# Kernel optimization log

Hardware: AMD Instinct MI355X
Metric: run time of the kernel (lower is better)

The kernel has to match this reference:

```python
import jax, jax.numpy as jnp
import numpy as np

BN_EPS = 1e-5

def batchnorm(x, gamma, beta):
    # training-mode BatchNorm1d over the row (node/sample) dimension
    mu = jnp.mean(x, axis=0)
    var = jnp.var(x, axis=0)
    return (x - mu) * jax.lax.rsqrt(var + BN_EPS) * gamma + beta

def gin_mean(h, src, dst, n):
    # DGL GINConv(apply_func=None, aggregator='mean', eps=0):
    # h_new = h + mean_{u in N(v)} h_u
    ones = jnp.ones((src.shape[0],), h.dtype)
    deg = jax.ops.segment_sum(ones, dst, num_segments=n)
    agg = jax.ops.segment_sum(h[src], dst, num_segments=n)
    return h + agg / jnp.maximum(deg, 1.0)[:, None]

def setup_inputs() -> dict:
    key = jax.random.key(0)
    ks = jax.random.split(key, 12)
    N, E, B, K = 10000, 160000, 64, 10
    DIN, D, DH = 20, 512, 256
    x = jax.random.normal(ks[0], (N, DIN), dtype=jnp.float32)
    edge_src = jax.random.randint(ks[1], (E,), 0, N, dtype=jnp.int32)
    edge_dst = jax.random.randint(ks[2], (E,), 0, N, dtype=jnp.int32)
    node2graph = jnp.sort(jax.random.randint(ks[3], (N,), 0, B, dtype=jnp.int32))
    pg_emb = jax.random.normal(ks[4], (B, D), dtype=jnp.float32)
    neigh_emb = jax.random.normal(ks[5], (B, K, D), dtype=jnp.float32)
    s = lambda i, shp: jax.random.normal(ks[i], shp, dtype=jnp.float32) * 0.02
    return dict(
        x=x, pg_emb=pg_emb, neigh_emb=neigh_emb,
        W_init=s(6, (DIN, D)), b_init=jnp.zeros((D,), jnp.float32),
        g1=jnp.ones((D,), jnp.float32), be1=jnp.zeros((D,), jnp.float32),
        g2=jnp.ones((D,), jnp.float32), be2=jnp.zeros((D,), jnp.float32),
        W_fc=s(7, (3 * D, DH)), b_fc=jnp.zeros((DH,), jnp.float32),
        W_fc2=s(8, (DH, DH)), b_fc2=jnp.zeros((DH,), jnp.float32),
        W_fc3=s(9, (DH, DH)), b_fc3=jnp.zeros((DH,), jnp.float32),
        W_fc4=s(10, (DH, 1)), b_fc4=jnp.zeros((1,), jnp.float32),
        gb=jnp.ones((DH,), jnp.float32), bb=jnp.zeros((DH,), jnp.float32),
        gb2=jnp.ones((DH,), jnp.float32), bb2=jnp.zeros((DH,), jnp.float32),
        gb3=jnp.ones((DH,), jnp.float32), bb3=jnp.zeros((DH,), jnp.float32),
        edge_src=edge_src, edge_dst=edge_dst, node2graph=node2graph,
    )

def reference(x, pg_emb, neigh_emb, W_init, b_init, g1, be1, g2, be2,
              W_fc, b_fc, W_fc2, b_fc2, W_fc3, b_fc3, W_fc4, b_fc4,
              gb, bb, gb2, bb2, gb3, bb3, edge_src, edge_dst, node2graph):
    N = x.shape[0]
    B, K, D = neigh_emb.shape
    # two GIN(mean) layers with BN+ReLU on the batched graph
    h = x @ W_init + b_init                                   # [N, 512]
    h = jax.nn.relu(batchnorm(gin_mean(h, edge_src, edge_dst, N), g1, be1))
    h = jax.nn.relu(batchnorm(gin_mean(h, edge_src, edge_dst, N), g2, be2))
    # dgl.mean_nodes: per-graph mean readout
    cnt = jax.ops.segment_sum(jnp.ones((N,), h.dtype), node2graph, num_segments=B)
    qemb = jax.ops.segment_sum(h, node2graph, num_segments=B) / jnp.maximum(cnt, 1.0)[:, None]
    a = jnp.concatenate([qemb, pg_emb], axis=1)               # [B, 2D]
    a = jnp.broadcast_to(a[:, None, :], (B, K, 2 * D))        # repeat per candidate
    b = jnp.concatenate([a, neigh_emb], axis=-1).reshape(B * K, 3 * D)
    H = jax.nn.relu(batchnorm(b @ W_fc + b_fc, gb, bb))
    H2 = jax.nn.relu(batchnorm(H @ W_fc2 + b_fc2, gb2, bb2))
    H3 = jax.nn.relu(batchnorm(H2 @ W_fc3 + b_fc3, gb3, bb3))
    pred = jax.nn.sigmoid(H3 @ W_fc4 + b_fc4)                 # [B*K, 1]
    return pred.reshape(B, K)
```

## Files before the change

kernel.cpp:

```cpp
#include <hip/hip_runtime.h>
#include <hip/hip_bf16.h>
#include <math.h>

#define N_NODES 10000
#define N_EDGES 160000
#define D 512
#define DIN 20
#define B 64
#define KC 10
#define DH 256
#define NROW (B*KC)
#define BN_EPS 1e-5f

__device__ __forceinline__ void f4acc(float4& a, const float4 v){
  a.x += v.x; a.y += v.y; a.z += v.z; a.w += v.w;
}
__device__ __forceinline__ void mk_affine(const float4 s, const float4 q, const float4 g,
                                          const float4 b, float4& sc, float4& sh){
  const float invN = 1.0f/(float)N_NODES;
  float mu, var, rs;
  mu = s.x*invN; var = q.x*invN - mu*mu; rs = rsqrtf(var+BN_EPS); sc.x = rs*g.x; sh.x = b.x - mu*sc.x;
  mu = s.y*invN; var = q.y*invN - mu*mu; rs = rsqrtf(var+BN_EPS); sc.y = rs*g.y; sh.y = b.y - mu*sc.y;
  mu = s.z*invN; var = q.z*invN - mu*mu; rs = rsqrtf(var+BN_EPS); sc.z = rs*g.z; sh.z = b.z - mu*sc.z;
  mu = s.w*invN; var = q.w*invN - mu*mu; rs = rsqrtf(var+BN_EPS); sc.w = rs*g.w; sh.w = b.w - mu*sc.w;
}
__device__ __forceinline__ float4 aff_relu(const float4 v, const float4 sc, const float4 sh){
  float4 o;
  o.x = fmaxf(fmaf(v.x, sc.x, sh.x), 0.0f);
  o.y = fmaxf(fmaf(v.y, sc.y, sh.y), 0.0f);
  o.z = fmaxf(fmaf(v.z, sc.z, sh.z), 0.0f);
  o.w = fmaxf(fmaf(v.w, sc.w, sh.w), 0.0f);
  return o;
}
__device__ __forceinline__ void bf_unpack(const uint4 u, float4& lo, float4& hi){
  lo.x = __uint_as_float(u.x << 16); lo.y = __uint_as_float(u.x & 0xffff0000u);
  lo.z = __uint_as_float(u.y << 16); lo.w = __uint_as_float(u.y & 0xffff0000u);
  hi.x = __uint_as_float(u.z << 16); hi.y = __uint_as_float(u.z & 0xffff0000u);
  hi.z = __uint_as_float(u.w << 16); hi.w = __uint_as_float(u.w & 0xffff0000u);
}
__device__ __forceinline__ unsigned bf_pack2(float a, float b){
  unsigned ua = __float_as_uint(a); ua = (ua + 0x7fffu + ((ua>>16)&1u)) >> 16;
  unsigned ub = __float_as_uint(b); ub = (ub + 0x7fffu + ((ub>>16)&1u)) & 0xffff0000u;
  return (ua & 0xffffu) | ub;
}
__device__ __forceinline__ unsigned short bf_pack1(float a){
  unsigned ua = __float_as_uint(a); return (unsigned short)((ua + 0x7fffu + ((ua>>16)&1u)) >> 16);
}

#define ZCOUNT 36352
#define Z4 (ZCOUNT/4)
#define D4 (N_NODES/4)
#define SETUP_ZBLK ((Z4 + D4 + 255)/256)
__global__ void setup_kernel(const int* __restrict__ n2g, int* __restrict__ gstart,
                             float* __restrict__ zbuf, int* __restrict__ degi){
  if (blockIdx.x == SETUP_ZBLK){
    int g = threadIdx.x;
    if (g > B) return;
    int lo = 0, hi = N_NODES;
    while (lo < hi){ int mid = (lo+hi)>>1; if (n2g[mid] < g) lo = mid+1; else hi = mid; }
    gstart[g] = lo;
    return;
  }
  int i4 = blockIdx.x*256 + threadIdx.x;
  if (i4 < Z4){
    ((float4*)zbuf)[i4] = make_float4(0.f,0.f,0.f,0.f);
  } else {
    int j = i4 - Z4;
    if (j < D4) ((int4*)degi)[j] = make_int4(0,0,0,0);
  }
}

__global__ void deg_kernel(const int* __restrict__ dst, int* __restrict__ degi, int E){
  int i = blockIdx.x*blockDim.x + threadIdx.x;
  if (i < E) atomicAdd(&degi[dst[i]], 1);
}

__global__ void scan_kernel(const int* __restrict__ degi, int* __restrict__ rowstart,
                            int* __restrict__ cursor){
  __shared__ int part[256];
  int t = threadIdx.x;
  const int PER = (N_NODES + 255)/256;
  int base = t*PER;
  int s = 0;
  for (int i = 0; i < PER; ++i){
    int idx = base+i;
    if (idx < N_NODES) s += degi[idx];
  }
  part[t] = s;
  __syncthreads();
  for (int off = 1; off < 256; off <<= 1){
    int v = (t >= off) ? part[t-off] : 0;
    __syncthreads();
    part[t] += v;
    __syncthreads();
  }
  int run = (t > 0) ? part[t-1] : 0;
  for (int i = 0; i < PER; ++i){
    int idx = base+i;
    if (idx < N_NODES){
      rowstart[idx] = run; cursor[idx] = run; run += degi[idx];
    }
  }
  if (t == 255) rowstart[N_NODES] = run;
}

__global__ void fill_kernel(const int* __restrict__ src, const int* __restrict__ dst,
                            int* __restrict__ cursor, int* __restrict__ csr, int E){
  int i = blockIdx.x*blockDim.x + threadIdx.x;
  if (i < E){
    int p = atomicAdd(&cursor[dst[i]], 1);
    csr[p] = src[i];
  }
}

#define IM_ROWS 8
__global__ __launch_bounds__(256)
void init_mm_kernel(const float* __restrict__ x, const float* __restrict__ W,
                    const float* __restrict__ b, unsigned short* __restrict__ hb){
  __shared__ float Ws[DIN][D];
  __shared__ float xs[IM_ROWS][DIN];
  int t = threadIdx.x;
  int r0 = blockIdx.x*IM_ROWS;
  for (int i = t; i < DIN*D; i += 256) Ws[i >> 9][i & (D-1)] = W[i];
  for (int i = t; i < IM_ROWS*DIN; i += 256) xs[i/DIN][i%DIN] = x[(size_t)r0*DIN + i];
  __syncthreads();
  float b0 = b[t], b1 = b[t+256];
  for (int rr = 0; rr < IM_ROWS; ++rr){
    float a0 = b0, a1 = b1;
    #pragma unroll
    for (int k = 0; k < DIN; ++k){
      float xv = xs[rr][k];
      a0 += xv*Ws[k][t];
      a1 += xv*Ws[k][t+256];
    }
    hb[(size_t)(r0+rr)*D + t]       = bf_pack1(a0);
    hb[(size_t)(r0+rr)*D + t + 256] = bf_pack1(a1);
  }
}

#define GWAVES 4
#define NPW 4
#define NWAVETOT (N_NODES/NPW)
template<bool FUSED>
__global__ __launch_bounds__(256, 2)
void gin_gather_kernel(const unsigned short* __restrict__ hb,
                       const int* __restrict__ rowstart,
                       const int* __restrict__ csr,
                       const float* __restrict__ pcsum, const float* __restrict__ pcsq,
                       const float* __restrict__ pgam, const float* __restrict__ pbet,
                       unsigned short* __restrict__ h2b,
                       float* __restrict__ csum, float* __restrict__ csq){
  __shared__ float red[GWAVES][1024];
  int lane = threadIdx.x & 63;
  int wave = threadIdx.x >> 6;
  int wid  = blockIdx.x*GWAVES + wave;
  const uint4* hb4 = (const uint4*)hb;
  float4 scA, shA, scB, shB;
  if (FUSED){
    mk_affine(((const float4*)pcsum)[2*lane],   ((const float4*)pcsq)[2*lane],
              ((const float4*)pgam)[2*lane],    ((const float4*)pbet)[2*lane],   scA, shA);
    mk_affine(((const float4*)pcsum)[2*lane+1], ((const float4*)pcsq)[2*lane+1],
              ((const float4*)pgam)[2*lane+1],  ((const float4*)pbet)[2*lane+1], scB, shB);
  }
  float4 sLo = make_float4(0,0,0,0), sHi = make_float4(0,0,0,0);
  float4 qLo = make_float4(0,0,0,0), qHi = make_float4(0,0,0,0);
  for (int nn = 0; nn < NPW; ++nn){
    int node = wid + nn*NWAVETOT;
    int start = rowstart[node], end = rowstart[node+1];
    float4 aLo = make_float4(0,0,0,0), aHi = make_float4(0,0,0,0);
    float4 bLo = make_float4(0,0,0,0), bHi = make_float4(0,0,0,0);
    for (int base = start; base < end; base += 64){
      int cnt = end - base; if (cnt > 64) cnt = 64;
      int myidx = (lane < cnt) ? csr[base+lane] : 0;
      int j = 0;
      for (; j+8 <= cnt; j += 8){
        uint4 u[8];
        #pragma unroll
        for (int k = 0; k < 8; ++k){
          int idx = __shfl(myidx, j+k, 64);
          u[k] = hb4[(size_t)idx*64 + lane];
        }
        #pragma unroll
        for (int k = 0; k < 8; ++k){
          float4 lo, hi; bf_unpack(u[k], lo, hi);
          if (FUSED){ lo = aff_relu(lo, scA, shA); hi = aff_relu(hi, scB, shB); }
          if (k & 1){ f4acc(bLo, lo); f4acc(bHi, hi); }
          else      { f4acc(aLo, lo); f4acc(aHi, hi); }
        }
      }
      for (; j < cnt; ++j){
        int idx = __shfl(myidx, j, 64);
        uint4 u0 = hb4[(size_t)idx*64 + lane];
        float4 lo, hi; bf_unpack(u0, lo, hi);
        if (FUSED){ lo = aff_relu(lo, scA, shA); hi = aff_relu(hi, scB, shB); }
        f4acc(aLo, lo); f4acc(aHi, hi);
      }
    }
    float inv = 1.0f/fmaxf((float)(end-start), 1.0f);
    uint4 us = hb4[(size_t)node*64 + lane];
    float4 hLo, hHi; bf_unpack(us, hLo, hHi);
    if (FUSED){ hLo = aff_relu(hLo, scA, shA); hHi = aff_relu(hHi, scB, shB); }
    float4 oLo, oHi;
    oLo.x = hLo.x + (aLo.x+bLo.x)*inv;  oLo.y = hLo.y + (aLo.y+bLo.y)*inv;
    oLo.z = hLo.z + (aLo.z+bLo.z)*inv;  oLo.w = hLo.w + (aLo.w+bLo.w)*inv;
    oHi.x = hHi.x + (aHi.x+bHi.x)*inv;  oHi.y = hHi.y + (aHi.y+bHi.y)*inv;
    oHi.z = hHi.z + (aHi.z+bHi.z)*inv;  oHi.w = hHi.w + (aHi.w+bHi.w)*inv;
    uint4 ou;
    ou.x = bf_pack2(oLo.x, oLo.y); ou.y = bf_pack2(oLo.z, oLo.w);
    ou.z = bf_pack2(oHi.x, oHi.y); ou.w = bf_pack2(oHi.z, oHi.w);
    ((uint4*)h2b)[(size_t)node*64 + lane] = ou;
    f4acc(sLo, oLo); f4acc(sHi, oHi);
    qLo.x += oLo.x*oLo.x; qLo.y += oLo.y*oLo.y; qLo.z += oLo.z*oLo.z; qLo.w += oLo.w*oLo.w;
    qHi.x += oHi.x*oHi.x; qHi.y += oHi.y*oHi.y; qHi.z += oHi.z*oHi.z; qHi.w += oHi.w*oHi.w;
  }
  float* my = red[wave];
  int c = 8*lane;
  *((float4*)&my[c])      = sLo;  *((float4*)&my[c+4])     = sHi;
  *((float4*)&my[512+c])  = qLo;  *((float4*)&my[512+c+4]) = qHi;
  __syncthreads();
  for (int e = threadIdx.x; e < 1024; e += 256){
    float v = red[0][e] + red[1][e] + red[2][e] + red[3][e];
    if (e < 512) atomicAdd(&csum[e], v);
    else         atomicAdd(&csq[e-512], v);
  }
}

__global__ void readout_kernel(const unsigned short* __restrict__ hb,
                               const float* __restrict__ csum, const float* __restrict__ csq,
                               const float* __restrict__ gam, const float* __restrict__ bet,
                               const int* __restrict__ gstart, float* __restrict__ qemb){
  __shared__ float red[4][512];
  int g = blockIdx.x, chunk = blockIdx.y;
  int lane = threadIdx.x & 63, wave = threadIdx.x >> 6;
  const uint4* hb4 = (const uint4*)hb;
  float4 scA, shA, scB, shB;
  mk_affine(((const float4*)csum)[2*lane],   ((const float4*)csq)[2*lane],
            ((const float4*)gam)[2*lane],    ((const float4*)bet)[2*lane],   scA, shA);
  mk_affine(((const float4*)csum)[2*lane+1], ((const float4*)csq)[2*lane+1],
            ((const float4*)gam)[2*lane+1],  ((const float4*)bet)[2*lane+1], scB, shB);
  int s = gstart[g], e = gstart[g+1];
  int rows = e - s;
  int per = (rows + 7)/8;
  int r0 = s + chunk*per;
  int r1 = r0 + per; if (r1 > e) r1 = e;
  float4 aLo = make_float4(0,0,0,0), aHi = make_float4(0,0,0,0);
  for (int r = r0 + wave; r < r1; r += 4){
    uint4 u = hb4[(size_t)r*64 + lane];
    float4 lo, hi; bf_unpack(u, lo, hi);
    lo = aff_relu(lo, scA, shA); hi = aff_relu(hi, scB, shB);
    f4acc(aLo, lo); f4acc(aHi, hi);
  }
  int c = 8*lane;
  *((float4*)&red[wave][c])   = aLo;
  *((float4*)&red[wave][c+4]) = aHi;
  __syncthreads();
  for (int e2 = threadIdx.x; e2 < 512; e2 += 256){
    float v = red[0][e2] + red[1][e2] + red[2][e2] + red[3][e2];
    atomicAdd(&qemb[(size_t)g*D + e2], v);
  }
}

#define F1_ROWS 8
#define F1_KS 256
#define F1_NS 6
__global__ __launch_bounds__(256)
void fc1_partial_kernel(const float* __restrict__ qemb, const int* __restrict__ gstart,
                        const float* __restrict__ pg, const float* __restrict__ neigh,
                        const float* __restrict__ W, float* __restrict__ part){
  __shared__ float brow[F1_ROWS][F1_KS];
  int t = threadIdx.x;
  int r0 = blockIdx.x*F1_ROWS;
  int k0 = blockIdx.y*F1_KS;
  for (int rr=0; rr<F1_ROWS; ++rr){
    int r = r0+rr;
    int g = r/KC, k = r - g*KC;
    int j = k0 + t;
    float v;
    if (j < D){
      float invc = 1.0f/fmaxf((float)(gstart[g+1]-gstart[g]), 1.0f);
      v = qemb[(size_t)g*D + j]*invc;
    } else if (j < 2*D){
      v = pg[(size_t)g*D + (j-D)];
    } else {
      v = neigh[((size_t)g*KC + k)*D + (j-2*D)];
    }
    brow[rr][t] = v;
  }
  __syncthreads();
  float acc[F1_ROWS] = {0.f,0.f,0.f,0.f,0.f,0.f,0.f,0.f};
  #pragma unroll 4
  for (int kk=0; kk<F1_KS; ++kk){
    float w = W[(size_t)(k0+kk)*DH + t];
    #pragma unroll
    for (int rr=0; rr<F1_ROWS; ++rr) acc[rr] += brow[rr][kk]*w;
  }
  for (int rr=0; rr<F1_ROWS; ++rr)
    part[((size_t)blockIdx.y*NROW + r0+rr)*DH + t] = acc[rr];
}

__global__ __launch_bounds__(256)
void reduce_stats_kernel(const float* __restrict__ part, const float* __restrict__ bias,
                         float* __restrict__ out, float* __restrict__ s, float* __restrict__ q,
                         int nslice){
  int t = threadIdx.x;
  int r0 = blockIdx.x*8;
  float bval = bias[t];
  float ls = 0.f, lq = 0.f;
  for (int rr = 0; rr < 8; ++rr){
    int r = r0+rr;
    float acc = bval;
    for (int sl = 0; sl < nslice; ++sl) acc += part[((size_t)sl*NROW + r)*DH + t];
    out[(size_t)r*DH + t] = acc;
    ls += acc; lq += acc*acc;
  }
  atomicAdd(&s[t], ls); atomicAdd(&q[t], lq);
}

#define FM_ROWS 4
#define FM_KS 128
#define FM_NS 2
__global__ __launch_bounds__(256)
void fc_mid_partial_kernel(const float* __restrict__ in, const float* __restrict__ ps,
                           const float* __restrict__ pq, const float* __restrict__ gamma,
                           const float* __restrict__ beta, const float* __restrict__ W,
                           float* __restrict__ part){
  __shared__ float row[FM_ROWS][FM_KS];
  int t = threadIdx.x;
  int r0 = blockIdx.x*FM_ROWS;
  int k0 = blockIdx.y*FM_KS;
  const float invM = 1.0f/(float)NROW;
  #pragma unroll
  for (int i = 0; i < 2; ++i){
    int idx = t + i*256;
    int rr = idx >> 7, kk = idx & 127;
    int c = k0 + kk;
    float mu = ps[c]*invM;
    float var = pq[c]*invM - mu*mu;
    float rs = rsqrtf(var + BN_EPS);
    float v = in[(size_t)(r0+rr)*DH + c];
    row[rr][kk] = fmaxf((v-mu)*rs*gamma[c] + beta[c], 0.0f);
  }
  __syncthreads();
  float acc[FM_ROWS] = {0.f,0.f,0.f,0.f};
  #pragma unroll 4
  for (int kk=0; kk<FM_KS; ++kk){
    float w = W[(size_t)(k0+kk)*DH + t];
    #pragma unroll
    for (int rr=0; rr<FM_ROWS; ++rr) acc[rr] += row[rr][kk]*w;
  }
  for (int rr=0; rr<FM_ROWS; ++rr)
    part[((size_t)blockIdx.y*NROW + r0+rr)*DH + t] = acc[rr];
}

__global__ void final_kernel(const float* __restrict__ G3, const float* __restrict__ ps,
                             const float* __restrict__ pq, const float* __restrict__ gamma,
                             const float* __restrict__ beta,
                             const float* __restrict__ w4, const float* __restrict__ b4,
                             float* __restrict__ out){
  int wave = threadIdx.x>>6, lane = threadIdx.x&63;
  int r = blockIdx.x*4 + wave;
  if (r >= NROW) return;
  const float invM = 1.0f/(float)NROW;
  float sum = 0.f;
  #pragma unroll
  for (int j=0;j<4;++j){
    int c = lane + 64*j;
    float mu = ps[c]*invM;
    float var = pq[c]*invM - mu*mu;
    float rs = rsqrtf(var+BN_EPS);
    float v = G3[(size_t)r*DH + c];
    v = fmaxf((v-mu)*rs*gamma[c]+beta[c], 0.0f);
    sum += v*w4[c];
  }
  #pragma unroll
  for (int off=32; off>0; off>>=1) sum += __shfl_down(sum, off, 64);
  if (lane==0){
    float z = sum + b4[0];
    out[r] = 1.0f/(1.0f + expf(-z));
  }
}

extern "C" void kernel_launch(void* const* d_in, const int* in_sizes, int n_in,
                              void* d_out, int out_size, void* d_ws, size_t ws_size,
                              hipStream_t stream) {
  const float* x        = (const float*)d_in[0];
  const float* pg_emb   = (const float*)d_in[1];
  const float* neigh    = (const float*)d_in[2];
  const float* W_init   = (const float*)d_in[3];
  const float* b_init   = (const float*)d_in[4];
  const float* g1       = (const float*)d_in[5];
  const float* be1      = (const float*)d_in[6];
  const float* g2       = (const float*)d_in[7];
  const float* be2      = (const float*)d_in[8];
  const float* W_fc     = (const float*)d_in[9];
  const float* b_fc     = (const float*)d_in[10];
  const float* W_fc2    = (const float*)d_in[11];
  const float* b_fc2    = (const float*)d_in[12];
  const float* W_fc3    = (const float*)d_in[13];
  const float* b_fc3    = (const float*)d_in[14];
  const float* W_fc4    = (const float*)d_in[15];
  const float* b_fc4    = (const float*)d_in[16];
  const float* gb       = (const float*)d_in[17];
  const float* bb       = (const float*)d_in[18];
  const float* gb2      = (const float*)d_in[19];
  const float* bb2      = (const float*)d_in[20];
  const float* gb3      = (const float*)d_in[21];
  const float* bb3      = (const float*)d_in[22];
  const int*   esrc     = (const int*)d_in[23];
  const int*   edst     = (const int*)d_in[24];
  const int*   n2g      = (const int*)d_in[25];
  float* out = (float*)d_out;

  float* ws = (float*)d_ws;
  size_t off = 0;
  unsigned short* hb0 = (unsigned short*)(ws + off); off += (size_t)N_NODES*D/2;
  unsigned short* hb1 = (unsigned short*)(ws + off); off += (size_t)N_NODES*D/2;
  unsigned short* hb2 = (unsigned short*)(ws + off); off += (size_t)N_NODES*D/2;
  float* zbase = ws + off;
  float* csum1 = ws + off; off += 512;
  float* csq1  = ws + off; off += 512;
  float* csum2 = ws + off; off += 512;
  float* csq2  = ws + off; off += 512;
  float* s1    = ws + off; off += 256;
  float* q1    = ws + off; off += 256;
  float* s2    = ws + off; off += 256;
  float* q2    = ws + off; off += 256;
  float* s3    = ws + off; off += 256;
  float* q3    = ws + off; off += 256;
  float* qemb  = ws + off; off += (size_t)B*D;
  float* G1   = ws + off; off += (size_t)NROW*DH;
  float* G2   = ws + off; off += (size_t)NROW*DH;
  float* G3   = ws + off; off += (size_t)NROW*DH;
  float* part = ws + off; off += (size_t)F1_NS*NROW*DH;
  int* degi     = (int*)(ws + off); off += N_NODES;
  int* rowstart = (int*)(ws + off); off += N_NODES + 1;
  int* cursor   = (int*)(ws + off); off += N_NODES;
  int* csr      = (int*)(ws + off); off += N_EDGES;
  int* gstart   = (int*)(ws + off); off += B + 1;
  (void)zbase;

  setup_kernel<<<SETUP_ZBLK+1, 256, 0, stream>>>(n2g, gstart, csum1, degi);
  deg_kernel<<<(N_EDGES+255)/256, 256, 0, stream>>>(edst, degi, N_EDGES);
  scan_kernel<<<1, 256, 0, stream>>>(degi, rowstart, cursor);
  fill_kernel<<<(N_EDGES+255)/256, 256, 0, stream>>>(esrc, edst, cursor, csr, N_EDGES);

  init_mm_kernel<<<N_NODES/IM_ROWS, 256, 0, stream>>>(x, W_init, b_init, hb0);

  gin_gather_kernel<false><<<NWAVETOT/GWAVES, 256, 0, stream>>>(
      hb0, rowstart, csr, nullptr, nullptr, nullptr, nullptr, hb1, csum1, csq1);
  gin_gather_kernel<true><<<NWAVETOT/GWAVES, 256, 0, stream>>>(
      hb1, rowstart, csr, csum1, csq1, g1, be1, hb2, csum2, csq2);

  readout_kernel<<<dim3(B, 8), 256, 0, stream>>>(hb2, csum2, csq2, g2, be2, gstart, qemb);

  fc1_partial_kernel<<<dim3(NROW/F1_ROWS, F1_NS), 256, 0, stream>>>(qemb, gstart, pg_emb, neigh, W_fc, part);
  reduce_stats_kernel<<<NROW/8, 256, 0, stream>>>(part, b_fc, G1, s1, q1, F1_NS);
  fc_mid_partial_kernel<<<dim3(NROW/FM_ROWS, FM_NS), 256, 0, stream>>>(G1, s1, q1, gb,  bb,  W_fc2, part);
  reduce_stats_kernel<<<NROW/8, 256, 0, stream>>>(part, b_fc2, G2, s2, q2, FM_NS);
  fc_mid_partial_kernel<<<dim3(NROW/FM_ROWS, FM_NS), 256, 0, stream>>>(G2, s2, q2, gb2, bb2, W_fc3, part);
  reduce_stats_kernel<<<NROW/8, 256, 0, stream>>>(part, b_fc3, G3, s3, q3, FM_NS);
  final_kernel<<<(NROW+3)/4, 256, 0, stream>>>(G3, s3, q3, gb3, bb3, W_fc4, b_fc4, out);
}
```

Baseline: 219.8 us.

## Merge pipeline stages into two cooperative persistent kernels with grid syncs

Replaces the chain of about fourteen small kernel launches with two cooperative persistent kernels of 512 blocks. Each kernel runs several phases (setup, degree count, scan, init matmul, CSR fill, gathers, readout, MLP layers) separated by grid-wide syncs, and the original multi-kernel path is kept as a fallback if the cooperative launch fails. The MLP middle layers also drop the split-K partial buffer by fusing bias and BN statistics into a full-K per-row computation, and the init matmul keeps weights in registers instead of shared memory. The aim is to remove launch gaps and tail idle time, at the cost of grid-sync overhead and lower parallelism in the small phases.

```diff
diff --git a/kernel.cpp b/kernel.cpp
--- a/kernel.cpp
+++ b/kernel.cpp
@@ -1,6 +1,9 @@
 #include <hip/hip_runtime.h>
+#include <hip/hip_cooperative_groups.h>
 #include <hip/hip_bf16.h>
 #include <math.h>
+
+namespace cg = cooperative_groups;
 
 #define N_NODES 10000
 #define N_EDGES 160000
@@ -12,6 +15,31 @@
 #define NROW (B*KC)
 #define BN_EPS 1e-5f
 
+#define ZCOUNT 36352
+#define Z4 (ZCOUNT/4)
+#define D4 (N_NODES/4)
+#define IM_ROWS 8
+#define IM_UNITS (N_NODES/IM_ROWS)
+#define GWAVES 4
+#define CGRID 512
+#define F1_NS 6
+#define F1_ROWS 8
+#define F1_KS 256
+
+struct P {
+  const float *x, *pg, *neigh, *Winit, *binit;
+  const float *g1, *be1, *g2, *be2;
+  const float *Wfc, *bfc, *W2, *b2, *W3, *b3, *W4, *b4;
+  const float *gbA, *bbA, *gbB, *bbB, *gbC, *bbC;
+  const int *esrc, *edst, *n2g;
+  unsigned short *hb0, *hb1, *hb2;
+  float *zbuf, *csum1, *csq1, *csum2, *csq2;
+  float *s1,*q1,*s2,*q2,*s3,*q3, *qemb;
+  float *G1,*G2,*G3,*part;
+  int *degi,*rowstart,*cursor,*csr,*gstart;
+  float *out;
+};
+
 __device__ __forceinline__ void f4acc(float4& a, const float4 v){
   a.x += v.x; a.y += v.y; a.z += v.z; a.w += v.w;
 }
@@ -47,45 +75,34 @@
   unsigned ua = __float_as_uint(a); return (unsigned short)((ua + 0x7fffu + ((ua>>16)&1u)) >> 16);
 }
 
-#define ZCOUNT 36352
-#define Z4 (ZCOUNT/4)
-#define D4 (N_NODES/4)
-#define SETUP_ZBLK ((Z4 + D4 + 255)/256)
-__global__ void setup_kernel(const int* __restrict__ n2g, int* __restrict__ gstart,
-                             float* __restrict__ zbuf, int* __restrict__ degi){
-  if (blockIdx.x == SETUP_ZBLK){
-    int g = threadIdx.x;
-    if (g > B) return;
+__device__ __forceinline__ void ph_setup(const P& p, int b, int nb, int t){
+  for (int i4 = b*256 + t; i4 < Z4 + D4; i4 += nb*256){
+    if (i4 < Z4) ((float4*)p.zbuf)[i4] = make_float4(0.f,0.f,0.f,0.f);
+    else         ((int4*)p.degi)[i4 - Z4] = make_int4(0,0,0,0);
+  }
+  if (b == 0 && t <= B){
     int lo = 0, hi = N_NODES;
-    while (lo < hi){ int mid = (lo+hi)>>1; if (n2g[mid] < g) lo = mid+1; else hi = mid; }
-    gstart[g] = lo;
-    return;
-  }
-  int i4 = blockIdx.x*256 + threadIdx.x;
-  if (i4 < Z4){
-    ((float4*)zbuf)[i4] = make_float4(0.f,0.f,0.f,0.f);
-  } else {
-    int j = i4 - Z4;
-    if (j < D4) ((int4*)degi)[j] = make_int4(0,0,0,0);
-  }
-}
-
-__global__ void deg_kernel(const int* __restrict__ dst, int* __restrict__ degi, int E){
-  int i = blockIdx.x*blockDim.x + threadIdx.x;
-  if (i < E) atomicAdd(&degi[dst[i]], 1);
-}
-
-__global__ void scan_kernel(const int* __restrict__ degi, int* __restrict__ rowstart,
-                            int* __restrict__ cursor){
-  __shared__ int part[256];
-  int t = threadIdx.x;
+    while (lo < hi){ int mid = (lo+hi)>>1; if (p.n2g[mid] < t) lo = mid+1; else hi = mid; }
+    p.gstart[t] = lo;
+  }
+}
+
+__device__ __forceinline__ void ph_deg(const P& p, int b, int nb, int t){
+  for (int e = b*256 + t; e < N_EDGES; e += nb*256) atomicAdd(&p.degi[p.edst[e]], 1);
+}
+
+__device__ __forceinline__ void ph_fill(const P& p, int b, int nb, int t){
+  for (int e = b*256 + t; e < N_EDGES; e += nb*256){
+    int pos = atomicAdd(&p.cursor[p.edst[e]], 1);
+    p.csr[pos] = p.esrc[e];
+  }
+}
+
+__device__ __forceinline__ void ph_scan(const P& p, int t, int* part){
   const int PER = (N_NODES + 255)/256;
   int base = t*PER;
   int s = 0;
-  for (int i = 0; i < PER; ++i){
-    int idx = base+i;
-    if (idx < N_NODES) s += degi[idx];
-  }
+  for (int i = 0; i < PER; ++i){ int idx = base+i; if (idx < N_NODES) s += p.degi[idx]; }
   part[t] = s;
   __syncthreads();
   for (int off = 1; off < 256; off <<= 1){
@@ -97,81 +114,60 @@
   int run = (t > 0) ? part[t-1] : 0;
   for (int i = 0; i < PER; ++i){
     int idx = base+i;
-    if (idx < N_NODES){
-      rowstart[idx] = run; cursor[idx] = run; run += degi[idx];
+    if (idx < N_NODES){ p.rowstart[idx] = run; p.cursor[idx] = run; run += p.degi[idx]; }
+  }
+  if (t == 255) p.rowstart[N_NODES] = run;
+}
+
+__device__ __forceinline__ void ph_init(const P& p, int u0, int ustride, int t, float* xs){
+  float wlo[DIN], whi[DIN];
+  #pragma unroll
+  for (int k = 0; k < DIN; ++k){ wlo[k] = p.Winit[k*D + t]; whi[k] = p.Winit[k*D + t + 256]; }
+  float b0 = p.binit[t], b1 = p.binit[t+256];
+  for (int unit = u0; unit < IM_UNITS; unit += ustride){
+    int r0 = unit*IM_ROWS;
+    __syncthreads();
+    for (int i = t; i < IM_ROWS*DIN; i += 256) xs[i] = p.x[(size_t)r0*DIN + i];
+    __syncthreads();
+    for (int rr = 0; rr < IM_ROWS; ++rr){
+      float a0 = b0, a1 = b1;
+      #pragma unroll
+      for (int k = 0; k < DIN; ++k){
+        float xv = xs[rr*DIN + k];
+        a0 += xv*wlo[k]; a1 += xv*whi[k];
+      }
+      p.hb0[(size_t)(r0+rr)*D + t]       = bf_pack1(a0);
+      p.hb0[(size_t)(r0+rr)*D + t + 256] = bf_pack1(a1);
     }
   }
-  if (t == 255) rowstart[N_NODES] = run;
-}
-
-__global__ void fill_kernel(const int* __restrict__ src, const int* __restrict__ dst,
-                            int* __restrict__ cursor, int* __restrict__ csr, int E){
-  int i = blockIdx.x*blockDim.x + threadIdx.x;
-  if (i < E){
-    int p = atomicAdd(&cursor[dst[i]], 1);
-    csr[p] = src[i];
-  }
-}
-
-#define IM_ROWS 8
-__global__ __launch_bounds__(256)
-void init_mm_kernel(const float* __restrict__ x, const float* __restrict__ W,
-                    const float* __restrict__ b, unsigned short* __restrict__ hb){
-  __shared__ float Ws[DIN][D];
-  __shared__ float xs[IM_ROWS][DIN];
-  int t = threadIdx.x;
-  int r0 = blockIdx.x*IM_ROWS;
-  for (int i = t; i < DIN*D; i += 256) Ws[i >> 9][i & (D-1)] = W[i];
-  for (int i = t; i < IM_ROWS*DIN; i += 256) xs[i/DIN][i%DIN] = x[(size_t)r0*DIN + i];
-  __syncthreads();
-  float b0 = b[t], b1 = b[t+256];
-  for (int rr = 0; rr < IM_ROWS; ++rr){
-    float a0 = b0, a1 = b1;
-    #pragma unroll
-    for (int k = 0; k < DIN; ++k){
-      float xv = xs[rr][k];
-      a0 += xv*Ws[k][t];
-      a1 += xv*Ws[k][t+256];
-    }
-    hb[(size_t)(r0+rr)*D + t]       = bf_pack1(a0);
-    hb[(size_t)(r0+rr)*D + t + 256] = bf_pack1(a1);
-  }
-}
-
-#define GWAVES 4
-#define NPW 4
-#define NWAVETOT (N_NODES/NPW)
+}
+
 template<bool FUSED>
-__global__ __launch_bounds__(256, 2)
-void gin_gather_kernel(const unsigned short* __restrict__ hb,
-                       const int* __restrict__ rowstart,
-                       const int* __restrict__ csr,
-                       const float* __restrict__ pcsum, const float* __restrict__ pcsq,
-                       const float* __restrict__ pgam, const float* __restrict__ pbet,
-                       unsigned short* __restrict__ h2b,
-                       float* __restrict__ csum, float* __restrict__ csq){
-  __shared__ float red[GWAVES][1024];
-  int lane = threadIdx.x & 63;
-  int wave = threadIdx.x >> 6;
-  int wid  = blockIdx.x*GWAVES + wave;
-  const uint4* hb4 = (const uint4*)hb;
+__device__ __forceinline__ void ph_gather(const P& p,
+    const unsigned short* __restrict__ hin, unsigned short* __restrict__ hout,
+    const float* pcs, const float* pcq, const float* pgm, const float* pbt,
+    float* cs, float* cq, int b, int nb, int t, float* red){
+  int lane = t & 63;
+  int wave = t >> 6;
+  int wid  = b*GWAVES + wave;
+  int tot  = nb*GWAVES;
+  const uint4* hb4 = (const uint4*)hin;
   float4 scA, shA, scB, shB;
   if (FUSED){
-    mk_affine(((const float4*)pcsum)[2*lane],   ((const float4*)pcsq)[2*lane],
-              ((const float4*)pgam)[2*lane],    ((const float4*)pbet)[2*lane],   scA, shA);
-    mk_affine(((const float4*)pcsum)[2*lane+1], ((const float4*)pcsq)[2*lane+1],
-              ((const float4*)pgam)[2*lane+1],  ((const float4*)pbet)[2*lane+1], scB, shB);
+    mk_affine(((const float4*)pcs)[2*lane],   ((const float4*)pcq)[2*lane],
+              ((const float4*)pgm)[2*lane],   ((const float4*)pbt)[2*lane],   scA, shA);
+    mk_affine(((const float4*)pcs)[2*lane+1], ((const float4*)pcq)[2*lane+1],
+              ((const float4*)pgm)[2*lane+1], ((const float4*)pbt)[2*lane+1], scB, shB);
   }
   float4 sLo = make_float4(0,0,0,0), sHi = make_float4(0,0,0,0);
   float4 qLo = make_float4(0,0,0,0), qHi = make_float4(0,0,0,0);
-  for (int nn = 0; nn < NPW; ++nn){
-    int node = wid + nn*NWAVETOT;
-    int start = rowstart[node], end = rowstart[node+1];
+  for (int node = wid; node < N_NODES; node += tot){
+    int start = p.rowstart[node], end = p.rowstart[node+1];
     float4 aLo = make_float4(0,0,0,0), aHi = make_float4(0,0,0,0);
     float4 bLo = make_float4(0,0,0,0), bHi = make_float4(0,0,0,0);
     for (int base = start; base < end; base += 64){
       int cnt = end - base; if (cnt > 64) cnt = 64;
-      int myidx = (lane < cnt) ? csr[base+lane] : 0;
+      int myidx = (lane < cnt) ? p.csr[base+lane] : 0;
       int j = 0;
       for (; j+8 <= cnt; j += 8){
         uint4 u[8];
@@ -208,37 +204,33 @@
     uint4 ou;
     ou.x = bf_pack2(oLo.x, oLo.y); ou.y = bf_pack2(oLo.z, oLo.w);
     ou.z = bf_pack2(oHi.x, oHi.y); ou.w = bf_pack2(oHi.z, oHi.w);
-    ((uint4*)h2b)[(size_t)node*64 + lane] = ou;
+    ((uint4*)hout)[(size_t)node*64 + lane] = ou;
     f4acc(sLo, oLo); f4acc(sHi, oHi);
     qLo.x += oLo.x*oLo.x; qLo.y += oLo.y*oLo.y; qLo.z += oLo.z*oLo.z; qLo.w += oLo.w*oLo.w;
     qHi.x += oHi.x*oHi.x; qHi.y += oHi.y*oHi.y; qHi.z += oHi.z*oHi.z; qHi.w += oHi.w*oHi.w;
   }
-  float* my = red[wave];
+  float* my = red + wave*1024;
   int c = 8*lane;
   *((float4*)&my[c])      = sLo;  *((float4*)&my[c+4])     = sHi;
   *((float4*)&my[512+c])  = qLo;  *((float4*)&my[512+c+4]) = qHi;
   __syncthreads();
-  for (int e = threadIdx.x; e < 1024; e += 256){
-    float v = red[0][e] + red[1][e] + red[2][e] + red[3][e];
-    if (e < 512) atomicAdd(&csum[e], v);
-    else         atomicAdd(&csq[e-512], v);
-  }
-}
-
-__global__ void readout_kernel(const unsigned short* __restrict__ hb,
-                               const float* __restrict__ csum, const float* __restrict__ csq,
-                               const float* __restrict__ gam, const float* __restrict__ bet,
-                               const int* __restrict__ gstart, float* __restrict__ qemb){
-  __shared__ float red[4][512];
-  int g = blockIdx.x, chunk = blockIdx.y;
-  int lane = threadIdx.x & 63, wave = threadIdx.x >> 6;
-  const uint4* hb4 = (const uint4*)hb;
+  for (int e = t; e < 1024; e += 256){
+    float v = red[e] + red[1024+e] + red[2048+e] + red[3072+e];
+    if (e < 512) atomicAdd(&cs[e], v);
+    else         atomicAdd(&cq[e-512], v);
+  }
+}
+
+__device__ __forceinline__ void ph_readout(const P& p, int b, int t, float* red){
+  int g = b >> 3, chunk = b & 7;
+  int lane = t & 63, wave = t >> 6;
+  const uint4* hb4 = (const uint4*)p.hb2;
   float4 scA, shA, scB, shB;
-  mk_affine(((const float4*)csum)[2*lane],   ((const float4*)csq)[2*lane],
-            ((const float4*)gam)[2*lane],    ((const float4*)bet)[2*lane],   scA, shA);
-  mk_affine(((const float4*)csum)[2*lane+1], ((const float4*)csq)[2*lane+1],
-            ((const float4*)gam)[2*lane+1],  ((const float4*)bet)[2*lane+1], scB, shB);
-  int s = gstart[g], e = gstart[g+1];
+  mk_affine(((const float4*)p.csum2)[2*lane],   ((const float4*)p.csq2)[2*lane],
+            ((const float4*)p.g2)[2*lane],      ((const float4*)p.be2)[2*lane],   scA, shA);
+  mk_affine(((const float4*)p.csum2)[2*lane+1], ((const float4*)p.csq2)[2*lane+1],
+            ((const float4*)p.g2)[2*lane+1],    ((const float4*)p.be2)[2*lane+1], scB, shB);
+  int s = p.gstart[g], e = p.gstart[g+1];
   int rows = e - s;
   int per = (rows + 7)/8;
   int r0 = s + chunk*per;
@@ -251,213 +243,252 @@
     f4acc(aLo, lo); f4acc(aHi, hi);
   }
   int c = 8*lane;
-  *((float4*)&red[wave][c])   = aLo;
-  *((float4*)&red[wave][c+4]) = aHi;
+  *((float4*)&red[wave*512 + c])     = aLo;
+  *((float4*)&red[wave*512 + c + 4]) = aHi;
   __syncthreads();
-  for (int e2 = threadIdx.x; e2 < 512; e2 += 256){
-    float v = red[0][e2] + red[1][e2] + red[2][e2] + red[3][e2];
-    atomicAdd(&qemb[(size_t)g*D + e2], v);
-  }
-}
-
-#define F1_ROWS 8
-#define F1_KS 256
-#define F1_NS 6
-__global__ __launch_bounds__(256)
-void fc1_partial_kernel(const float* __restrict__ qemb, const int* __restrict__ gstart,
-                        const float* __restrict__ pg, const float* __restrict__ neigh,
-                        const float* __restrict__ W, float* __restrict__ part){
-  __shared__ float brow[F1_ROWS][F1_KS];
-  int t = threadIdx.x;
-  int r0 = blockIdx.x*F1_ROWS;
-  int k0 = blockIdx.y*F1_KS;
-  for (int rr=0; rr<F1_ROWS; ++rr){
+  for (int e2 = t; e2 < 512; e2 += 256){
+    float v = red[e2] + red[512+e2] + red[1024+e2] + red[1536+e2];
+    atomicAdd(&p.qemb[(size_t)g*D + e2], v);
+  }
+}
+
+__device__ __forceinline__ void ph_fc1(const P& p, int u, int t, float* brow){
+  int rb = u % 80, ks = u / 80;
+  int r0 = rb*F1_ROWS, k0 = ks*F1_KS;
+  for (int rr = 0; rr < F1_ROWS; ++rr){
     int r = r0+rr;
     int g = r/KC, k = r - g*KC;
     int j = k0 + t;
     float v;
     if (j < D){
-      float invc = 1.0f/fmaxf((float)(gstart[g+1]-gstart[g]), 1.0f);
-      v = qemb[(size_t)g*D + j]*invc;
+      float invc = 1.0f/fmaxf((float)(p.gstart[g+1]-p.gstart[g]), 1.0f);
+      v = p.qemb[(size_t)g*D + j]*invc;
     } else if (j < 2*D){
-      v = pg[(size_t)g*D + (j-D)];
+      v = p.pg[(size_t)g*D + (j-D)];
     } else {
-      v = neigh[((size_t)g*KC + k)*D + (j-2*D)];
+      v = p.neigh[((size_t)g*KC + k)*D + (j-2*D)];
     }
-    brow[rr][t] = v;
+    brow[rr*F1_KS + t] = v;
   }
   __syncthreads();
   float acc[F1_ROWS] = {0.f,0.f,0.f,0.f,0.f,0.f,0.f,0.f};
   #pragma unroll 4
-  for (int kk=0; kk<F1_KS; ++kk){
-    float w = W[(size_t)(k0+kk)*DH + t];
+  for (int kk = 0; kk < F1_KS; ++kk){
+    float w = p.Wfc[(size_t)(k0+kk)*DH + t];
     #pragma unroll
-    for (int rr=0; rr<F1_ROWS; ++rr) acc[rr] += brow[rr][kk]*w;
-  }
-  for (int rr=0; rr<F1_ROWS; ++rr)
-    part[((size_t)blockIdx.y*NROW + r0+rr)*DH + t] = acc[rr];
-}
-
-__global__ __launch_bounds__(256)
-void reduce_stats_kernel(const float* __restrict__ part, const float* __restrict__ bias,
-                         float* __restrict__ out, float* __restrict__ s, float* __restrict__ q,
-                         int nslice){
-  int t = threadIdx.x;
-  int r0 = blockIdx.x*8;
+    for (int rr = 0; rr < F1_ROWS; ++rr) acc[rr] += brow[rr*F1_KS + kk]*w;
+  }
+  for (int rr = 0; rr < F1_ROWS; ++rr)
+    p.part[((size_t)ks*NROW + r0+rr)*DH + t] = acc[rr];
+}
+
+__device__ __forceinline__ void ph_reduce(const float* part, const float* bias,
+                                          float* outG, float* s, float* q, int u, int t){
+  int r0 = u*8;
   float bval = bias[t];
   float ls = 0.f, lq = 0.f;
   for (int rr = 0; rr < 8; ++rr){
     int r = r0+rr;
     float acc = bval;
-    for (int sl = 0; sl < nslice; ++sl) acc += part[((size_t)sl*NROW + r)*DH + t];
-    out[(size_t)r*DH + t] = acc;
+    for (int sl = 0; sl < F1_NS; ++sl) acc += part[((size_t)sl*NROW + r)*DH + t];
+    outG[(size_t)r*DH + t] = acc;
     ls += acc; lq += acc*acc;
   }
   atomicAdd(&s[t], ls); atomicAdd(&q[t], lq);
 }
 
-#define FM_ROWS 4
-#define FM_KS 128
-#define FM_NS 2
-__global__ __launch_bounds__(256)
-void fc_mid_partial_kernel(const float* __restrict__ in, const float* __restrict__ ps,
-                           const float* __restrict__ pq, const float* __restrict__ gamma,
-                           const float* __restrict__ beta, const float* __restrict__ W,
-                           float* __restrict__ part){
-  __shared__ float row[FM_ROWS][FM_KS];
-  int t = threadIdx.x;
-  int r0 = blockIdx.x*FM_ROWS;
-  int k0 = blockIdx.y*FM_KS;
+__device__ __forceinline__ void ph_fcmid(const float* in, const float* ps, const float* pq,
+    const float* gamma, const float* beta, const float* W, const float* bias,
+    float* outG, float* s, float* q, int u, int t, float* row){
+  int r0 = u*4;
   const float invM = 1.0f/(float)NROW;
   #pragma unroll
-  for (int i = 0; i < 2; ++i){
+  for (int i = 0; i < 4; ++i){
     int idx = t + i*256;
-    int rr = idx >> 7, kk = idx & 127;
-    int c = k0 + kk;
-    float mu = ps[c]*invM;
-    float var = pq[c]*invM - mu*mu;
+    int rr = idx >> 8, kk = idx & 255;
+    float mu = ps[kk]*invM;
+    float var = pq[kk]*invM - mu*mu;
     float rs = rsqrtf(var + BN_EPS);
-    float v = in[(size_t)(r0+rr)*DH + c];
-    row[rr][kk] = fmaxf((v-mu)*rs*gamma[c] + beta[c], 0.0f);
+    float v = in[(size_t)(r0+rr)*DH + kk];
+    row[rr*DH + kk] = fmaxf((v-mu)*rs*gamma[kk] + beta[kk], 0.0f);
   }
   __syncthreads();
-  float acc[FM_ROWS] = {0.f,0.f,0.f,0.f};
+  float bv = bias[t];
+  float a0 = bv, a1 = bv, a2 = bv, a3 = bv;
   #pragma unroll 4
-  for (int kk=0; kk<FM_KS; ++kk){
-    float w = W[(size_t)(k0+kk)*DH + t];
-    #pragma unroll
-    for (int rr=0; rr<FM_ROWS; ++rr) acc[rr] += row[rr][kk]*w;
-  }
-  for (int rr=0; rr<FM_ROWS; ++rr)
-    part[((size_t)blockIdx.y*NROW + r0+rr)*DH + t] = acc[rr];
-}
-
-__global__ void final_kernel(const float* __restrict__ G3, const float* __restrict__ ps,
-                             const float* __restrict__ pq, const float* __restrict__ gamma,
-                             const float* __restrict__ beta,
-                             const float* __restrict__ w4, const float* __restrict__ b4,
-                             float* __restrict__ out){
-  int wave = threadIdx.x>>6, lane = threadIdx.x&63;
-  int r = blockIdx.x*4 + wave;
-  if (r >= NROW) return;
+  for (int kk = 0; kk < DH; ++kk){
+    float w = W[(size_t)kk*DH + t];
+    a0 += row[0*DH+kk]*w; a1 += row[1*DH+kk]*w;
+    a2 += row[2*DH+kk]*w; a3 += row[3*DH+kk]*w;
+  }
+  outG[(size_t)(r0+0)*DH + t] = a0;
+  outG[(size_t)(r0+1)*DH + t] = a1;
+  outG[(size_t)(r0+2)*DH + t] = a2;
+  outG[(size_t)(r0+3)*DH + t] = a3;
+  float ls = a0+a1+a2+a3;
+  float lq = a0*a0 + a1*a1 + a2*a2 + a3*a3;
+  atomicAdd(&s[t], ls); atomicAdd(&q[t], lq);
+}
+
+__device__ __forceinline__ void ph_final(const P& p, int u, int t){
+  int wave = t>>6, lane = t&63;
+  int r = u*4 + wave;
   const float invM = 1.0f/(float)NROW;
   float sum = 0.f;
   #pragma unroll
-  for (int j=0;j<4;++j){
+  for (int j = 0; j < 4; ++j){
     int c = lane + 64*j;
-    float mu = ps[c]*invM;
-    float var = pq[c]*invM - mu*mu;
+    float mu = p.s3[c]*invM;
+    float var = p.q3[c]*invM - mu*mu;
     float rs = rsqrtf(var+BN_EPS);
-    float v = G3[(size_t)r*DH + c];
-    v = fmaxf((v-mu)*rs*gamma[c]+beta[c], 0.0f);
-    sum += v*w4[c];
+    float v = p.G3[(size_t)r*DH + c];
+    v = fmaxf((v-mu)*rs*p.gbC[c] + p.bbC[c], 0.0f);
+    sum += v*p.W4[c];
   }
   #pragma unroll
-  for (int off=32; off>0; off>>=1) sum += __shfl_down(sum, off, 64);
-  if (lane==0){
-    float z = sum + b4[0];
-    out[r] = 1.0f/(1.0f + expf(-z));
-  }
-}
+  for (int off = 32; off > 0; off >>= 1) sum += __shfl_down(sum, off, 64);
+  if (lane == 0){
+    float z = sum + p.b4[0];
+    p.out[r] = 1.0f/(1.0f + expf(-z));
+  }
+}
+
+__global__ __launch_bounds__(256, 2)
+void coopA(P p){
+  cg::grid_group grid = cg::this_grid();
+  __shared__ float lds[4096];
+  int b = blockIdx.x, nb = gridDim.x, t = threadIdx.x;
+  ph_setup(p, b, nb, t);
+  grid.sync();
+  ph_deg(p, b, nb, t);
+  grid.sync();
+  if (b == 0) ph_scan(p, t, (int*)lds);
+  else        ph_init(p, b-1, nb-1, t, lds);
+  grid.sync();
+  ph_fill(p, b, nb, t);
+  grid.sync();
+  ph_gather<false>(p, p.hb0, p.hb1, nullptr,nullptr,nullptr,nullptr,
+                   p.csum1, p.csq1, b, nb, t, lds);
+}
+
+__global__ __launch_bounds__(256, 2)
+void coopB(P p){
+  cg::grid_group grid = cg::this_grid();
+  __shared__ float lds[4096];
+  int b = blockIdx.x, nb = gridDim.x, t = threadIdx.x;
+  ph_gather<true>(p, p.hb1, p.hb2, p.csum1, p.csq1, p.g1, p.be1,
+                  p.csum2, p.csq2, b, nb, t, lds);
+  grid.sync();
+  ph_readout(p, b, t, lds);
+  grid.sync();
+  if (b < 480) ph_fc1(p, b, t, lds);
+  grid.sync();
+  if (b < 80) ph_reduce(p.part, p.bfc, p.G1, p.s1, p.q1, b, t);
+  grid.sync();
+  if (b < 160) ph_fcmid(p.G1, p.s1, p.q1, p.gbA, p.bbA, p.W2, p.b2, p.G2, p.s2, p.q2, b, t, lds);
+  grid.sync();
+  if (b < 160) ph_fcmid(p.G2, p.s2, p.q2, p.gbB, p.bbB, p.W3, p.b3, p.G3, p.s3, p.q3, b, t, lds);
+  grid.sync();
+  if (b < 160) ph_final(p, b, t);
+}
+
+__global__ __launch_bounds__(256,2) void k_setup(P p){ ph_setup(p, blockIdx.x, gridDim.x, threadIdx.x); }
+__global__ __launch_bounds__(256,2) void k_deg(P p){ ph_deg(p, blockIdx.x, gridDim.x, threadIdx.x); }
+__global__ __launch_bounds__(256,2) void k_scan(P p){ __shared__ int il[256]; ph_scan(p, threadIdx.x, il); }
+__global__ __launch_bounds__(256,2) void k_init(P p){ __shared__ float xs[IM_ROWS*DIN]; ph_init(p, blockIdx.x, gridDim.x, threadIdx.x, xs); }
+__global__ __launch_bounds__(256,2) void k_fill(P p){ ph_fill(p, blockIdx.x, gridDim.x, threadIdx.x); }
+__global__ __launch_bounds__(256,2) void k_g1(P p){ __shared__ float red[4096];
+  ph_gather<false>(p, p.hb0, p.hb1, nullptr,nullptr,nullptr,nullptr, p.csum1, p.csq1,
+                   blockIdx.x, gridDim.x, threadIdx.x, red); }
+__global__ __launch_bounds__(256,2) void k_g2(P p){ __shared__ float red[4096];
+  ph_gather<true>(p, p.hb1, p.hb2, p.csum1, p.csq1, p.g1, p.be1, p.csum2, p.csq2,
+                  blockIdx.x, gridDim.x, threadIdx.x, red); }
+__global__ __launch_bounds__(256,2) void k_readout(P p){ __shared__ float red[2048]; ph_readout(p, blockIdx.x, threadIdx.x, red); }
+__global__ __launch_bounds__(256,2) void k_fc1(P p){ __shared__ float brow[2048]; ph_fc1(p, blockIdx.x, threadIdx.x, brow); }
+__global__ __launch_bounds__(256,2) void k_reduce(P p){ ph_reduce(p.part, p.bfc, p.G1, p.s1, p.q1, blockIdx.x, threadIdx.x); }
+__global__ __launch_bounds__(256,2) void k_fc2(P p){ __shared__ float row[1024];
+  ph_fcmid(p.G1, p.s1, p.q1, p.gbA, p.bbA, p.W2, p.b2, p.G2, p.s2, p.q2, blockIdx.x, threadIdx.x, row); }
+__global__ __launch_bounds__(256,2) void k_fc3(P p){ __shared__ float row[1024];
+  ph_fcmid(p.G2, p.s2, p.q2, p.gbB, p.bbB, p.W3, p.b3, p.G3, p.s3, p.q3, blockIdx.x, threadIdx.x, row); }
+__global__ __launch_bounds__(256,2) void k_final(P p){ ph_final(p, blockIdx.x, threadIdx.x); }
 
 extern "C" void kernel_launch(void* const* d_in, const int* in_sizes, int n_in,
                               void* d_out, int out_size, void* d_ws, size_t ws_size,
                               hipStream_t stream) {
-  const float* x        = (const float*)d_in[0];
-  const float* pg_emb   = (const float*)d_in[1];
-  const float* neigh    = (const float*)d_in[2];
-  const float* W_init   = (const float*)d_in[3];
-  const float* b_init   = (const float*)d_in[4];
-  const float* g1       = (const float*)d_in[5];
-  const float* be1      = (const float*)d_in[6];
-  const float* g2       = (const float*)d_in[7];
-  const float* be2      = (const float*)d_in[8];
-  const float* W_fc     = (const float*)d_in[9];
-  const float* b_fc     = (const float*)d_in[10];
-  const float* W_fc2    = (const float*)d_in[11];
-  const float* b_fc2    = (const float*)d_in[12];
-  const float* W_fc3    = (const float*)d_in[13];
-  const float* b_fc3    = (const float*)d_in[14];
-  const float* W_fc4    = (const float*)d_in[15];
-  const float* b_fc4    = (const float*)d_in[16];
-  const float* gb       = (const float*)d_in[17];
-  const float* bb       = (const float*)d_in[18];
-  const float* gb2      = (const float*)d_in[19];
-  const float* bb2      = (const float*)d_in[20];
-  const float* gb3      = (const float*)d_in[21];
-  const float* bb3      = (const float*)d_in[22];
-  const int*   esrc     = (const int*)d_in[23];
-  const int*   edst     = (const int*)d_in[24];
-  const int*   n2g      = (const int*)d_in[25];
-  float* out = (float*)d_out;
+  P p;
+  p.x     = (const float*)d_in[0];
+  p.pg    = (const float*)d_in[1];
+  p.neigh = (const float*)d_in[2];
+  p.Winit = (const float*)d_in[3];
+  p.binit = (const float*)d_in[4];
+  p.g1    = (const float*)d_in[5];
+  p.be1   = (const float*)d_in[6];
+  p.g2    = (const float*)d_in[7];
+  p.be2   = (const float*)d_in[8];
+  p.Wfc   = (const float*)d_in[9];
+  p.bfc   = (const float*)d_in[10];
+  p.W2    = (const float*)d_in[11];
+  p.b2    = (const float*)d_in[12];
+  p.W3    = (const float*)d_in[13];
+  p.b3    = (const float*)d_in[14];
+  p.W4    = (const float*)d_in[15];
+  p.b4    = (const float*)d_in[16];
+  p.gbA   = (const float*)d_in[17];
+  p.bbA   = (const float*)d_in[18];
+  p.gbB   = (const float*)d_in[19];
+  p.bbB   = (const float*)d_in[20];
+  p.gbC   = (const float*)d_in[21];
+  p.bbC   = (const float*)d_in[22];
+  p.esrc  = (const int*)d_in[23];
+  p.edst  = (const int*)d_in[24];
+  p.n2g   = (const int*)d_in[25];
+  p.out   = (float*)d_out;
 
   float* ws = (float*)d_ws;
   size_t off = 0;
-  unsigned short* hb0 = (unsigned short*)(ws + off); off += (size_t)N_NODES*D/2;
-  unsigned short* hb1 = (unsigned short*)(ws + off); off += (size_t)N_NODES*D/2;
-  unsigned short* hb2 = (unsigned short*)(ws + off); off += (size_t)N_NODES*D/2;
-  float* zbase = ws + off;
-  float* csum1 = ws + off; off += 512;
-  float* csq1  = ws + off; off += 512;
-  float* csum2 = ws + off; off += 512;
-  float* csq2  = ws + off; off += 512;
-  float* s1    = ws + off; off += 256;
-  float* q1    = ws + off; off += 256;
-  float* s2    = ws + off; off += 256;
-  float* q2    = ws + off; off += 256;
-  float* s3    = ws + off; off += 256;
-  float* q3    = ws + off; off += 256;
-  float* qemb  = ws + off; off += (size_t)B*D;
-  float* G1   = ws + off; off += (size_t)NROW*DH;
-  float* G2   = ws + off; off += (size_t)NROW*DH;
-  float* G3   = ws + off; off += (size_t)NROW*DH;
-  float* part = ws + off; off += (size_t)F1_NS*NROW*DH;
-  int* degi     = (int*)(ws + off); off += N_NODES;
-  int* rowstart = (int*)(ws + off); off += N_NODES + 1;
-  int* cursor   = (int*)(ws + off); off += N_NODES;
-  int* csr      = (int*)(ws + off); off += N_EDGES;
-  int* gstart   = (int*)(ws + off); off += B + 1;
-  (void)zbase;
-
-  setup_kernel<<<SETUP_ZBLK+1, 256, 0, stream>>>(n2g, gstart, csum1, degi);
-  deg_kernel<<<(N_EDGES+255)/256, 256, 0, stream>>>(edst, degi, N_EDGES);
-  scan_kernel<<<1, 256, 0, stream>>>(degi, rowstart, cursor);
-  fill_kernel<<<(N_EDGES+255)/256, 256, 0, stream>>>(esrc, edst, cursor, csr, N_EDGES);
-
-  init_mm_kernel<<<N_NODES/IM_ROWS, 256, 0, stream>>>(x, W_init, b_init, hb0);
-
-  gin_gather_kernel<false><<<NWAVETOT/GWAVES, 256, 0, stream>>>(
-      hb0, rowstart, csr, nullptr, nullptr, nullptr, nullptr, hb1, csum1, csq1);
-  gin_gather_kernel<true><<<NWAVETOT/GWAVES, 256, 0, stream>>>(
-      hb1, rowstart, csr, csum1, csq1, g1, be1, hb2, csum2, csq2);
-
-  readout_kernel<<<dim3(B, 8), 256, 0, stream>>>(hb2, csum2, csq2, g2, be2, gstart, qemb);
-
-  fc1_partial_kernel<<<dim3(NROW/F1_ROWS, F1_NS), 256, 0, stream>>>(qemb, gstart, pg_emb, neigh, W_fc, part);
-  reduce_stats_kernel<<<NROW/8, 256, 0, stream>>>(part, b_fc, G1, s1, q1, F1_NS);
-  fc_mid_partial_kernel<<<dim3(NROW/FM_ROWS, FM_NS), 256, 0, stream>>>(G1, s1, q1, gb,  bb,  W_fc2, part);
-  reduce_stats_kernel<<<NROW/8, 256, 0, stream>>>(part, b_fc2, G2, s2, q2, FM_NS);
-  fc_mid_partial_kernel<<<dim3(NROW/FM_ROWS, FM_NS), 256, 0, stream>>>(G2, s2, q2, gb2, bb2, W_fc3, part);
-  reduce_stats_kernel<<<NROW/8, 256, 0, stream>>>(part, b_fc3, G3, s3, q3, FM_NS);
-  final_kernel<<<(NROW+3)/4, 256, 0, stream>>>(G3, s3, q3, gb3, bb3, W_fc4, b_fc4, out);
-}
+  p.hb0 = (unsigned short*)(ws + off); off += (size_t)N_NODES*D/2;
+  p.hb1 = (unsigned short*)(ws + off); off += (size_t)N_NODES*D/2;
+  p.hb2 = (unsigned short*)(ws + off); off += (size_t)N_NODES*D/2;
+  p.zbuf  = ws + off;
+  p.csum1 = ws + off; off += 512;
+  p.csq1  = ws + off; off += 512;
+  p.csum2 = ws + off; off += 512;
+  p.csq2  = ws + off; off += 512;
+  p.s1    = ws + off; off += 256;
+  p.q1    = ws + off; off += 256;
+  p.s2    = ws + off; off += 256;
+  p.q2    = ws + off; off += 256;
+  p.s3    = ws + off; off += 256;
+  p.q3    = ws + off; off += 256;
+  p.qemb  = ws + off; off += (size_t)B*D;
+  p.G1   = ws + off; off += (size_t)NROW*DH;
+  p.G2   = ws + off; off += (size_t)NROW*DH;
+  p.G3   = ws + off; off += (size_t)NROW*DH;
+  p.part = ws + off; off += (size_t)F1_NS*NROW*DH;
+  p.degi     = (int*)(ws + off); off += N_NODES;
+  p.rowstart = (int*)(ws + off); off += N_NODES + 1;
+  p.cursor   = (int*)(ws + off); off += N_NODES;
+  p.csr      = (int*)(ws + off); off += N_EDGES;
+  p.gstart   = (int*)(ws + off); off += B + 1;
+
+  void* args[] = { &p };
+  hipError_t e1 = hipLaunchCooperativeKernel((void*)coopA, dim3(CGRID), dim3(256), args, 0, stream);
+  if (e1 != hipSuccess){
+    k_setup<<<64, 256, 0, stream>>>(p);
+    k_deg<<<625, 256, 0, stream>>>(p);
+    k_scan<<<1, 256, 0, stream>>>(p);
+    k_init<<<625, 256, 0, stream>>>(p);
+    k_fill<<<625, 256, 0, stream>>>(p);
+    k_g1<<<625, 256, 0, stream>>>(p);
+  }
+  hipError_t e2 = hipLaunchCooperativeKernel((void*)coopB, dim3(CGRID), dim3(256), args, 0, stream);
+  if (e2 != hipSuccess){
+    k_g2<<<625, 256, 0, stream>>>(p);
+    k_readout<<<512, 256, 0, stream>>>(p);
+    k_fc1<<<480, 256, 0, stream>>>(p);
+    k_reduce<<<80, 256, 0, stream>>>(p);
+    k_fc2<<<160, 256, 0, stream>>>(p);
+    k_fc3<<<160, 256, 0, stream>>>(p);
+    k_final<<<160, 256, 0, stream>>>(p);
+  }
+}
```

New measurement: 763.0 us. 3.47x slower.
